# Kernel tuning notes

Measured on AMD Instinct MI355X. Metric: run time of the kernel, lower is better.

Reference implementation:

```python
import jax, jax.numpy as jnp
import numpy as np

WH, WW = 7, 7
N = WH * WW
DIM = 128
NH = 4
HD = DIM // NH
B_IMG, NW = 64, 64
B_ = B_IMG * NW

def _relative_position_index():
    ch = np.arange(WH)
    cw = np.arange(WW)
    coords = np.stack(np.meshgrid(ch, cw, indexing='ij'))  # (2, Wh, Ww)
    coords = coords.reshape(2, -1)  # (2, N)
    rel = coords[:, :, None] - coords[:, None, :]  # (2, N, N)
    rel = rel.transpose(1, 2, 0)  # (N, N, 2)
    rel[:, :, 0] += WH - 1
    rel[:, :, 1] += WW - 1
    rel[:, :, 0] *= 2 * WW - 1
    return jnp.asarray(rel.sum(-1), dtype=jnp.int32)  # (N, N)

REL_IDX = _relative_position_index()

def setup_inputs() -> dict:
    key = jax.random.key(0)
    k1, k2, k3, k4, k5 = jax.random.split(key, 5)
    return {
        'x': jax.random.normal(k1, (B_, N, DIM), dtype=jnp.float32),
        'mask': jax.random.normal(k2, (NW, N, N), dtype=jnp.float32),
        'qkv_w': jax.random.normal(k3, (3 * DIM, DIM), dtype=jnp.float32) * 0.02,
        'qkv_b': jax.random.normal(k4, (3 * DIM,), dtype=jnp.float32) * 0.02,
        'rel_table': jax.random.normal(k5, ((2 * WH - 1) * (2 * WW - 1), NH), dtype=jnp.float32) * 0.02,
    }

def reference(x, mask, qkv_w, qkv_b, rel_table):
    B_tot, n, c = x.shape
    scale = HD ** (-0.5)
    # qkv projection; torch split order is (nH, hD, qkv) innermost-to-outermost
    qkv = x @ qkv_w.T + qkv_b                      # (B_, N, 3C)
    qkv = qkv.reshape(B_tot, n, NH, HD, 3)
    q = jnp.transpose(qkv[..., 0], (0, 2, 1, 3))   # (B_, nH, N, hD)
    k = jnp.transpose(qkv[..., 1], (0, 2, 1, 3))
    v = jnp.transpose(qkv[..., 2], (0, 2, 1, 3))
    attn = jnp.einsum('bhnd,bhmd->bhnm', q, k) * scale  # (B_, nH, N, N)
    bias = jnp.transpose(rel_table[REL_IDX.reshape(-1)].reshape(n, n, NH), (2, 0, 1))
    attn = attn + bias[None]
    nW = mask.shape[0]
    attn = attn.reshape(B_tot // nW, nW, NH, n, n) + mask[None, :, None]
    attn = attn.reshape(B_tot, NH, n, n)
    attn = jax.nn.softmax(attn, axis=-1)
    out = jnp.einsum('bhnm,bhmd->bhnd', attn, v)   # (B_, nH, N, hD)
    return jnp.transpose(out, (0, 2, 1, 3)).reshape(B_tot, n, c)
```

## Files before the change

### kernel.cpp

```cpp
#include <hip/hip_runtime.h>


typedef short bf16x8 __attribute__((ext_vector_type(8)));
typedef float f32x4 __attribute__((ext_vector_type(4)));

#define DEVI __device__ __forceinline__

DEVI unsigned short f2b(float f) {
    unsigned u = __builtin_bit_cast(unsigned, f);
    u += 0x7fffu + ((u >> 16) & 1u);
    return (unsigned short)(u >> 16);
}

struct __align__(16) Smem {
    unsigned short qk[2][4][64][32];
    union {
        unsigned short xs[64][136];
        unsigned short vt[4][32][72];
    } b;
};

__global__ void prep_kernel(const float* __restrict__ w, unsigned short* __restrict__ o) {
    int i = blockIdx.x * 256 + threadIdx.x;
    float4 v = ((const float4*)w)[i];
    ((ushort4*)o)[i] = make_ushort4(f2b(v.x), f2b(v.y), f2b(v.z), f2b(v.w));
}

template <bool USE_WS>
__global__ __launch_bounds__(512, 6) void wattn_kernel(
    const float* __restrict__ xg, const float* __restrict__ maskg,
    const float* __restrict__ qkvw, const unsigned short* __restrict__ wb,
    const float* __restrict__ qkvb, const float* __restrict__ relt,
    float* __restrict__ outg)
{
    __shared__ Smem sm;
    const int tid  = threadIdx.x;
    const int lane = tid & 63;
    const int wv   = tid >> 6;
    const int h    = wv & 3;
    const int half = wv >> 2;
    const int lr   = lane & 15;
    const int lq   = lane >> 4;
    const int bI   = blockIdx.x;

    const float* xb = xg + (size_t)bI * 6272;
    #pragma unroll
    for (int it = 0; it < 4; ++it) {
        int i = it * 512 + tid;
        if (i < 1568) {
            float4 v = ((const float4*)xb)[i];
            int row = i >> 5, col = (i & 31) << 2;
            *(ushort4*)&sm.b.xs[row][col] =
                make_ushort4(f2b(v.x), f2b(v.y), f2b(v.z), f2b(v.w));
        }
    }
    if (tid < 480) {
        int idx = tid << 2;
        *(ushort4*)&sm.b.xs[49 + (idx >> 7)][idx & 127] = make_ushort4(0, 0, 0, 0);
    }
    __syncthreads();

    bf16x8 af[4][2];
    #pragma unroll
    for (int ks = 0; ks < 4; ++ks)
        #pragma unroll
        for (int mtl = 0; mtl < 2; ++mtl)
            af[ks][mtl] = *(const bf16x8*)&sm.b.xs[(half * 2 + mtl) * 16 + lr][ks * 32 + lq * 8];
    __syncthreads();

    unsigned short* sbase = (unsigned short*)&sm;
    #pragma unroll
    for (int j = 0; j < 6; ++j) {
        const int c   = (h * 6 + j) * 16 + lr;
        const float bc = qkvb[c];
        const int rem = j * 16 + lr;
        const int dd  = rem / 3, s = rem % 3;
        const float mulv = (s == 0) ? 0.17677669529663687f : 1.0f;
        f32x4 acc[2];
        acc[0] = f32x4{0.f, 0.f, 0.f, 0.f};
        acc[1] = f32x4{0.f, 0.f, 0.f, 0.f};
        #pragma unroll
        for (int ks = 0; ks < 4; ++ks) {
            bf16x8 bf;
            if constexpr (USE_WS) {
                bf = *(const bf16x8*)&wb[c * 128 + ks * 32 + lq * 8];
            } else {
                const float4* wp = (const float4*)(qkvw + c * 128 + ks * 32 + lq * 8);
                float4 w0 = wp[0], w1 = wp[1];
                bf16x8 t;
                t[0] = (short)f2b(w0.x); t[1] = (short)f2b(w0.y);
                t[2] = (short)f2b(w0.z); t[3] = (short)f2b(w0.w);
                t[4] = (short)f2b(w1.x); t[5] = (short)f2b(w1.y);
                t[6] = (short)f2b(w1.z); t[7] = (short)f2b(w1.w);
                bf = t;
            }
            #pragma unroll
            for (int mtl = 0; mtl < 2; ++mtl)
                acc[mtl] = __builtin_amdgcn_mfma_f32_16x16x32_bf16(af[ks][mtl], bf, acc[mtl], 0, 0, 0);
        }
        #pragma unroll
        for (int mtl = 0; mtl < 2; ++mtl)
            #pragma unroll
            for (int r = 0; r < 4; ++r) {
                int m = (half * 2 + mtl) * 16 + lq * 4 + r;
                int soff = (s == 2) ? (16384 + (h * 32 + dd) * 72 + m)
                                    : (s * 8192 + h * 2048 + m * 32 + dd);
                sbase[soff] = f2b((acc[mtl][r] + bc) * mulv);
            }
    }
    __syncthreads();

    bf16x8 kf[4];
    #pragma unroll
    for (int t = 0; t < 4; ++t)
        kf[t] = *(const bf16x8*)&sm.qk[1][h][t * 16 + lr][lq * 8];

    const float* mw = maskg + (size_t)(bI & 63) * 2401;
    float* ob = outg + (size_t)bI * 6272;
    const int src0 = ((lq & 1) * 2) * 16 + lr;
    const int src1 = src0 + 16;
    const bool up  = (lq >= 2);

    #pragma unroll
    for (int bl = 0; bl < 2; ++bl) {
        const int mt = half * 2 + bl;
        bf16x8 qf = *(const bf16x8*)&sm.qk[0][h][mt * 16 + lr][lq * 8];

        f32x4 st[4];
        #pragma unroll
        for (int a = 0; a < 4; ++a) {
            f32x4 z = f32x4{0.f, 0.f, 0.f, 0.f};
            st[a] = __builtin_amdgcn_mfma_f32_16x16x32_bf16(kf[a], qf, z, 0, 0, 0);
        }

        const int m  = mt * 16 + lr;
        const int mi = m < 48 ? m : 48;
        const int md = mi / 7, mm = mi - md * 7;
        #pragma unroll
        for (int a = 0; a < 4; ++a)
            #pragma unroll
            for (int r = 0; r < 4; ++r) {
                int n  = a * 16 + lq * 4 + r;
                int ni = n < 48 ? n : 48;
                int nd = ni / 7, nm = ni - nd * 7;
                int ridx = (md - nd + 6) * 13 + (mm - nm + 6);
                float v = st[a][r] + relt[ridx * 4 + h] + mw[mi * 49 + ni];
                st[a][r] = (n < 49) ? v : -1e30f;
            }

        float mx = -3.4e38f;
        #pragma unroll
        for (int a = 0; a < 4; ++a)
            #pragma unroll
            for (int r = 0; r < 4; ++r) mx = fmaxf(mx, st[a][r]);
        mx = fmaxf(mx, __shfl_xor(mx, 16));
        mx = fmaxf(mx, __shfl_xor(mx, 32));
        float sum = 0.f;
        #pragma unroll
        for (int a = 0; a < 4; ++a)
            #pragma unroll
            for (int r = 0; r < 4; ++r) {
                float e = __expf(st[a][r] - mx);
                st[a][r] = e;
                sum += e;
            }
        sum += __shfl_xor(sum, 16);
        sum += __shfl_xor(sum, 32);
        const float inv = 1.f / sum;

        unsigned pk[4][2];
        #pragma unroll
        for (int a = 0; a < 4; ++a) {
            pk[a][0] = (unsigned)f2b(st[a][0] * inv) | ((unsigned)f2b(st[a][1] * inv) << 16);
            pk[a][1] = (unsigned)f2b(st[a][2] * inv) | ((unsigned)f2b(st[a][3] * inv) << 16);
        }

        f32x4 o[2];
        o[0] = f32x4{0.f, 0.f, 0.f, 0.f};
        o[1] = f32x4{0.f, 0.f, 0.f, 0.f};
        #pragma unroll
        for (int kt = 0; kt < 2; ++kt) {
            unsigned ea0 = (unsigned)__shfl((int)pk[2 * kt][0], src0);
            unsigned ea1 = (unsigned)__shfl((int)pk[2 * kt][1], src0);
            unsigned ea2 = (unsigned)__shfl((int)pk[2 * kt][0], src1);
            unsigned ea3 = (unsigned)__shfl((int)pk[2 * kt][1], src1);
            unsigned eb0 = (unsigned)__shfl((int)pk[2 * kt + 1][0], src0);
            unsigned eb1 = (unsigned)__shfl((int)pk[2 * kt + 1][1], src0);
            unsigned eb2 = (unsigned)__shfl((int)pk[2 * kt + 1][0], src1);
            unsigned eb3 = (unsigned)__shfl((int)pk[2 * kt + 1][1], src1);
            union { unsigned u[4]; bf16x8 v; } pu;
            pu.u[0] = up ? eb0 : ea0;
            pu.u[1] = up ? eb1 : ea1;
            pu.u[2] = up ? eb2 : ea2;
            pu.u[3] = up ? eb3 : ea3;
            #pragma unroll
            for (int dt = 0; dt < 2; ++dt) {
                bf16x8 vf = *(const bf16x8*)&sm.b.vt[h][dt * 16 + lr][kt * 32 + lq * 8];
                o[dt] = __builtin_amdgcn_mfma_f32_16x16x32_bf16(vf, pu.v, o[dt], 0, 0, 0);
            }
        }

        if (m < 49) {
            #pragma unroll
            for (int dt = 0; dt < 2; ++dt) {
                float4 v = make_float4(o[dt][0], o[dt][1], o[dt][2], o[dt][3]);
                *(float4*)&ob[m * 128 + h * 32 + dt * 16 + lq * 4] = v;
            }
        }
    }
}

extern "C" void kernel_launch(void* const* d_in, const int* in_sizes, int n_in,
                              void* d_out, int out_size, void* d_ws, size_t ws_size,
                              hipStream_t stream) {
    const float* x    = (const float*)d_in[0];
    const float* mask = (const float*)d_in[1];
    const float* qkvw = (const float*)d_in[2];
    const float* qkvb = (const float*)d_in[3];
    const float* relt = (const float*)d_in[4];
    float* out = (float*)d_out;

    const bool use_ws = (d_ws != nullptr) && (ws_size >= 49152 * sizeof(unsigned short));
    if (use_ws) {
        unsigned short* wbf = (unsigned short*)d_ws;
        prep_kernel<<<48, 256, 0, stream>>>(qkvw, wbf);
        wattn_kernel<true><<<4096, 512, 0, stream>>>(x, mask, qkvw, wbf, qkvb, relt, out);
    } else {
        wattn_kernel<false><<<4096, 512, 0, stream>>>(x, mask, qkvw, nullptr, qkvb, relt, out);
    }
}
```

Before: 310.7 us.

## Precompute combined mask+bias table and permuted pre-scaled weights in prep kernel

The prep kernel now reorders the QKV weight rows into q/k/v-contiguous order, folds the softmax scale into the q weights and bias, and builds a per-window, per-head table that sums the mask and the relative-position bias (stored transposed). The main kernel loads this combined table straight into the MFMA accumulator, so the index arithmetic and two gathers per score disappear. Q/K/V stores become simpler, with vectorized V-transpose writes. In exchange it needs about 2.5 MB of workspace and a larger prep launch, and the combined table is read with a strided gather instead of contiguous mask rows.

```diff
diff --git a/kernel.cpp b/kernel.cpp
--- a/kernel.cpp
+++ b/kernel.cpp
@@ -10,6 +10,37 @@
     unsigned u = __builtin_bit_cast(unsigned, f);
     u += 0x7fffu + ((u >> 16) & 1u);
     return (unsigned short)(u >> 16);
+}
+
+#define WS_BIAS_OFF 98304
+#define WS_COMB_OFF 131072
+#define WS_NEED     (131072u + 64u * 4u * 2401u * 4u)
+
+__global__ void prep_kernel(const float* __restrict__ qkvw, const float* __restrict__ qkvb,
+                            const float* __restrict__ maskg, const float* __restrict__ relt,
+                            unsigned short* __restrict__ wb, float* __restrict__ bb,
+                            float* __restrict__ comb) {
+    const int blk = blockIdx.x;
+    const int tid = threadIdx.x;
+    if (blk < 384) {
+        const int s = blk >> 7, r7 = blk & 127, h = r7 >> 5, d = r7 & 31;
+        const int c = h * 96 + d * 3 + s;
+        const float mul = (s == 0) ? 0.17677669529663687f : 1.0f;
+        if (tid < 128) wb[blk * 128 + tid] = f2b(qkvw[c * 128 + tid] * mul);
+        if (tid == 128) bb[blk] = qkvb[c] * mul;
+    } else {
+        const int wh = blk - 384;
+        const int w = wh >> 2, h = wh & 3;
+        const float* mw = maskg + w * 2401;
+        float* cbp = comb + wh * 2401;
+        for (int i = tid; i < 2401; i += 256) {
+            int n = i / 49, m = i - n * 49;
+            int md = m / 7, mm = m - md * 7;
+            int nd = n / 7, nm = n - nd * 7;
+            int ridx = (md - nd + 6) * 13 + (mm - nm + 6);
+            cbp[i] = mw[m * 49 + n] + relt[ridx * 4 + h];
+        }
+    }
 }
 
 struct __align__(16) Smem {
@@ -20,16 +51,11 @@
     } b;
 };
 
-__global__ void prep_kernel(const float* __restrict__ w, unsigned short* __restrict__ o) {
-    int i = blockIdx.x * 256 + threadIdx.x;
-    float4 v = ((const float4*)w)[i];
-    ((ushort4*)o)[i] = make_ushort4(f2b(v.x), f2b(v.y), f2b(v.z), f2b(v.w));
-}
-
 template <bool USE_WS>
 __global__ __launch_bounds__(512, 6) void wattn_kernel(
-    const float* __restrict__ xg, const float* __restrict__ maskg,
-    const float* __restrict__ qkvw, const unsigned short* __restrict__ wb,
+    const float* __restrict__ xg, const unsigned short* __restrict__ wb,
+    const float* __restrict__ bb, const float* __restrict__ comb,
+    const float* __restrict__ maskg, const float* __restrict__ qkvw,
     const float* __restrict__ qkvb, const float* __restrict__ relt,
     float* __restrict__ outg)
 {
@@ -68,23 +94,52 @@
             af[ks][mtl] = *(const bf16x8*)&sm.b.xs[(half * 2 + mtl) * 16 + lr][ks * 32 + lq * 8];
     __syncthreads();
 
-    unsigned short* sbase = (unsigned short*)&sm;
-    #pragma unroll
-    for (int j = 0; j < 6; ++j) {
-        const int c   = (h * 6 + j) * 16 + lr;
-        const float bc = qkvb[c];
-        const int rem = j * 16 + lr;
-        const int dd  = rem / 3, s = rem % 3;
-        const float mulv = (s == 0) ? 0.17677669529663687f : 1.0f;
-        f32x4 acc[2];
-        acc[0] = f32x4{0.f, 0.f, 0.f, 0.f};
-        acc[1] = f32x4{0.f, 0.f, 0.f, 0.f};
-        #pragma unroll
-        for (int ks = 0; ks < 4; ++ks) {
-            bf16x8 bf;
-            if constexpr (USE_WS) {
-                bf = *(const bf16x8*)&wb[c * 128 + ks * 32 + lq * 8];
-            } else {
+    if constexpr (USE_WS) {
+        #pragma unroll
+        for (int j = 0; j < 6; ++j) {
+            const int s     = j >> 1;
+            const int dhalf = j & 1;
+            const int cp    = s * 128 + h * 32 + dhalf * 16 + lr;
+            const int dd    = dhalf * 16 + lr;
+            const float bc  = bb[cp];
+            f32x4 acc[2];
+            acc[0] = f32x4{0.f, 0.f, 0.f, 0.f};
+            acc[1] = f32x4{0.f, 0.f, 0.f, 0.f};
+            #pragma unroll
+            for (int ks = 0; ks < 4; ++ks) {
+                bf16x8 bf = *(const bf16x8*)&wb[cp * 128 + ks * 32 + lq * 8];
+                #pragma unroll
+                for (int mtl = 0; mtl < 2; ++mtl)
+                    acc[mtl] = __builtin_amdgcn_mfma_f32_16x16x32_bf16(af[ks][mtl], bf, acc[mtl], 0, 0, 0);
+            }
+            #pragma unroll
+            for (int mtl = 0; mtl < 2; ++mtl) {
+                const int m0 = (half * 2 + mtl) * 16 + lq * 4;
+                if (s == 2) {
+                    *(ushort4*)&sm.b.vt[h][dd][m0] =
+                        make_ushort4(f2b(acc[mtl][0] + bc), f2b(acc[mtl][1] + bc),
+                                     f2b(acc[mtl][2] + bc), f2b(acc[mtl][3] + bc));
+                } else {
+                    #pragma unroll
+                    for (int r = 0; r < 4; ++r)
+                        sm.qk[s][h][m0 + r][dd] = f2b(acc[mtl][r] + bc);
+                }
+            }
+        }
+    } else {
+        unsigned short* sbase = (unsigned short*)&sm;
+        #pragma unroll
+        for (int j = 0; j < 6; ++j) {
+            const int c = (h * 6 + j) * 16 + lr;
+            const float bc = qkvb[c];
+            const int rem = j * 16 + lr;
+            const int dd = rem / 3, s = rem % 3;
+            const float mulv = (s == 0) ? 0.17677669529663687f : 1.0f;
+            f32x4 acc[2];
+            acc[0] = f32x4{0.f, 0.f, 0.f, 0.f};
+            acc[1] = f32x4{0.f, 0.f, 0.f, 0.f};
+            #pragma unroll
+            for (int ks = 0; ks < 4; ++ks) {
                 const float4* wp = (const float4*)(qkvw + c * 128 + ks * 32 + lq * 8);
                 float4 w0 = wp[0], w1 = wp[1];
                 bf16x8 t;
@@ -92,21 +147,20 @@
                 t[2] = (short)f2b(w0.z); t[3] = (short)f2b(w0.w);
                 t[4] = (short)f2b(w1.x); t[5] = (short)f2b(w1.y);
                 t[6] = (short)f2b(w1.z); t[7] = (short)f2b(w1.w);
-                bf = t;
+                #pragma unroll
+                for (int mtl = 0; mtl < 2; ++mtl)
+                    acc[mtl] = __builtin_amdgcn_mfma_f32_16x16x32_bf16(af[ks][mtl], t, acc[mtl], 0, 0, 0);
             }
             #pragma unroll
             for (int mtl = 0; mtl < 2; ++mtl)
-                acc[mtl] = __builtin_amdgcn_mfma_f32_16x16x32_bf16(af[ks][mtl], bf, acc[mtl], 0, 0, 0);
-        }
-        #pragma unroll
-        for (int mtl = 0; mtl < 2; ++mtl)
-            #pragma unroll
-            for (int r = 0; r < 4; ++r) {
-                int m = (half * 2 + mtl) * 16 + lq * 4 + r;
-                int soff = (s == 2) ? (16384 + (h * 32 + dd) * 72 + m)
-                                    : (s * 8192 + h * 2048 + m * 32 + dd);
-                sbase[soff] = f2b((acc[mtl][r] + bc) * mulv);
-            }
+                #pragma unroll
+                for (int r = 0; r < 4; ++r) {
+                    int m = (half * 2 + mtl) * 16 + lq * 4 + r;
+                    int soff = (s == 2) ? (16384 + (h * 32 + dd) * 72 + m)
+                                        : (s * 8192 + h * 2048 + m * 32 + dd);
+                    sbase[soff] = f2b((acc[mtl][r] + bc) * mulv);
+                }
+        }
     }
     __syncthreads();
 
@@ -115,7 +169,8 @@
     for (int t = 0; t < 4; ++t)
         kf[t] = *(const bf16x8*)&sm.qk[1][h][t * 16 + lr][lq * 8];
 
-    const float* mw = maskg + (size_t)(bI & 63) * 2401;
+    const float* cwh = comb + (size_t)((bI & 63) * 4 + h) * 2401;
+    const float* mw  = maskg + (size_t)(bI & 63) * 2401;
     float* ob = outg + (size_t)bI * 6272;
     const int src0 = ((lq & 1) * 2) * 16 + lr;
     const int src1 = src0 + 16;
@@ -124,29 +179,43 @@
     #pragma unroll
     for (int bl = 0; bl < 2; ++bl) {
         const int mt = half * 2 + bl;
-        bf16x8 qf = *(const bf16x8*)&sm.qk[0][h][mt * 16 + lr][lq * 8];
-
-        f32x4 st[4];
-        #pragma unroll
-        for (int a = 0; a < 4; ++a) {
-            f32x4 z = f32x4{0.f, 0.f, 0.f, 0.f};
-            st[a] = __builtin_amdgcn_mfma_f32_16x16x32_bf16(kf[a], qf, z, 0, 0, 0);
-        }
-
         const int m  = mt * 16 + lr;
         const int mi = m < 48 ? m : 48;
-        const int md = mi / 7, mm = mi - md * 7;
-        #pragma unroll
-        for (int a = 0; a < 4; ++a)
-            #pragma unroll
-            for (int r = 0; r < 4; ++r) {
-                int n  = a * 16 + lq * 4 + r;
-                int ni = n < 48 ? n : 48;
-                int nd = ni / 7, nm = ni - nd * 7;
-                int ridx = (md - nd + 6) * 13 + (mm - nm + 6);
-                float v = st[a][r] + relt[ridx * 4 + h] + mw[mi * 49 + ni];
-                st[a][r] = (n < 49) ? v : -1e30f;
-            }
+
+        f32x4 st[4];
+        if constexpr (USE_WS) {
+            f32x4 cc[4];
+            #pragma unroll
+            for (int a = 0; a < 4; ++a)
+                #pragma unroll
+                for (int r = 0; r < 4; ++r) {
+                    int n = a * 16 + lq * 4 + r;
+                    cc[a][r] = (n < 49) ? cwh[n * 49 + mi] : -1e30f;
+                }
+            bf16x8 qf = *(const bf16x8*)&sm.qk[0][h][m][lq * 8];
+            #pragma unroll
+            for (int a = 0; a < 4; ++a)
+                st[a] = __builtin_amdgcn_mfma_f32_16x16x32_bf16(kf[a], qf, cc[a], 0, 0, 0);
+        } else {
+            bf16x8 qf = *(const bf16x8*)&sm.qk[0][h][m][lq * 8];
+            #pragma unroll
+            for (int a = 0; a < 4; ++a) {
+                f32x4 z = f32x4{0.f, 0.f, 0.f, 0.f};
+                st[a] = __builtin_amdgcn_mfma_f32_16x16x32_bf16(kf[a], qf, z, 0, 0, 0);
+            }
+            const int md = mi / 7, mm = mi - md * 7;
+            #pragma unroll
+            for (int a = 0; a < 4; ++a)
+                #pragma unroll
+                for (int r = 0; r < 4; ++r) {
+                    int n = a * 16 + lq * 4 + r;
+                    int ni = n < 48 ? n : 48;
+                    int nd = ni / 7, nm = ni - nd * 7;
+                    int ridx = (md - nd + 6) * 13 + (mm - nm + 6);
+                    float v = st[a][r] + relt[ridx * 4 + h] + mw[mi * 49 + ni];
+                    st[a][r] = (n < 49) ? v : -1e30f;
+                }
+        }
 
         float mx = -3.4e38f;
         #pragma unroll
@@ -220,12 +289,13 @@
     const float* relt = (const float*)d_in[4];
     float* out = (float*)d_out;
 
-    const bool use_ws = (d_ws != nullptr) && (ws_size >= 49152 * sizeof(unsigned short));
-    if (use_ws) {
+    if (d_ws != nullptr && ws_size >= (size_t)WS_NEED) {
         unsigned short* wbf = (unsigned short*)d_ws;
-        prep_kernel<<<48, 256, 0, stream>>>(qkvw, wbf);
-        wattn_kernel<true><<<4096, 512, 0, stream>>>(x, mask, qkvw, wbf, qkvb, relt, out);
+        float* bbf  = (float*)((char*)d_ws + WS_BIAS_OFF);
+        float* comb = (float*)((char*)d_ws + WS_COMB_OFF);
+        prep_kernel<<<640, 256, 0, stream>>>(qkvw, qkvb, mask, relt, wbf, bbf, comb);
+        wattn_kernel<true><<<4096, 512, 0, stream>>>(x, wbf, bbf, comb, mask, qkvw, qkvb, relt, out);
     } else {
-        wattn_kernel<false><<<4096, 512, 0, stream>>>(x, mask, qkvw, nullptr, qkvb, relt, out);
+        wattn_kernel<false><<<4096, 512, 0, stream>>>(x, nullptr, nullptr, nullptr, mask, qkvw, qkvb, relt, out);
     }
 }
```

After: 266.7 us. 14.2% less time.
